# Optimization experiments

Measured on AMD Instinct MI355X. Metric: run time of the kernel, lower is better.

Reference implementation:

```python
import jax, jax.numpy as jnp
import numpy as np

N_NODES = 50000
N_EDGES = 800000
D_FEAT = 128
HIDDEN = 128
N_CLASSES = 40


def setup_inputs() -> dict:
    key = jax.random.key(0)
    ks = jax.random.split(key, 8)
    s = 1.0 / np.sqrt(D_FEAT)
    return {
        "x": jax.random.normal(ks[0], (N_NODES, D_FEAT), jnp.float32),
        "edge_index": jax.random.randint(ks[1], (2, N_EDGES), 0, N_NODES, jnp.int64),
        "Wl0": jax.random.normal(ks[2], (D_FEAT, HIDDEN), jnp.float32) * s,
        "bl0": jnp.zeros((HIDDEN,), jnp.float32),
        "Wr0": jax.random.normal(ks[3], (D_FEAT, HIDDEN), jnp.float32) * s,
        "Wl1": jax.random.normal(ks[4], (HIDDEN, HIDDEN), jnp.float32) * s,
        "bl1": jnp.zeros((HIDDEN,), jnp.float32),
        "Wr1": jax.random.normal(ks[5], (HIDDEN, HIDDEN), jnp.float32) * s,
        "Wl2": jax.random.normal(ks[6], (HIDDEN, N_CLASSES), jnp.float32) * s,
        "bl2": jnp.zeros((N_CLASSES,), jnp.float32),
        "Wr2": jax.random.normal(ks[7], (HIDDEN, N_CLASSES), jnp.float32) * s,
    }


def _sage_conv(x, src, dst, Wl, bl, Wr):
    # PyG SAGEConv (mean aggr): out = lin_l(mean_{j in N(i)} x_j) + lin_r(x_i)
    msg_sum = jax.ops.segment_sum(x[src], dst, num_segments=N_NODES)  # [N, d]
    deg = jax.ops.segment_sum(jnp.ones((src.shape[0],), x.dtype), dst, num_segments=N_NODES)
    mean = msg_sum / jnp.clip(deg, 1.0)[:, None]
    return mean @ Wl + bl + x @ Wr


def reference(x, edge_index, Wl0, bl0, Wr0, Wl1, bl1, Wr1, Wl2, bl2, Wr2):
    src, dst = edge_index[0], edge_index[1]
    h = jax.nn.relu(_sage_conv(x, src, dst, Wl0, bl0, Wr0))
    h = jax.nn.relu(_sage_conv(h, src, dst, Wl1, bl1, Wr1))
    h = jax.nn.relu(_sage_conv(h, src, dst, Wl2, bl2, Wr2))
    # dropout is identity in eval mode
    return jax.nn.log_softmax(h, axis=1)
```

## Files before the change

### kernel.cpp

```cpp
#include <hip/hip_runtime.h>
#include <cstdint>
#include <cstddef>
#include <cmath>

#define N_NODES 50000
#define N_EDGES 800000
#define D_FEAT 128
#define HIDDEN 128
#define N_CLASSES 40

typedef _Float16 half8 __attribute__((ext_vector_type(8)));
typedef _Float16 half4 __attribute__((ext_vector_type(4)));
typedef float f32x4 __attribute__((ext_vector_type(4)));

#define EDGE_BLOCKS 3125
#define CVT_BLOCKS 6250


__global__ __launch_bounds__(256) void k_build(const int* __restrict__ dst, int* __restrict__ deg,
                                               unsigned short* __restrict__ rank,
                                               const float* __restrict__ x, _Float16* __restrict__ xh,
                                               const float* __restrict__ Wl0, const float* __restrict__ Wr0, _Float16* __restrict__ Wc0,
                                               const float* __restrict__ Wl1, const float* __restrict__ Wr1, _Float16* __restrict__ Wc1,
                                               const float* __restrict__ Wl2, const float* __restrict__ Wr2, _Float16* __restrict__ Wc2) {
    int bid = blockIdx.x;
    if (bid < EDGE_BLOCKS) {
        int e = bid * 256 + threadIdx.x;
        int r = atomicAdd(&deg[dst[e]], 1);
        rank[e] = (unsigned short)r;
        return;
    }
    bid -= EDGE_BLOCKS;
    if (bid < CVT_BLOCKS) {
        int i = bid * 256 + threadIdx.x;
        float4 v = *(const float4*)(x + (size_t)i * 4);
        half4 o;
        o[0] = (_Float16)v.x; o[1] = (_Float16)v.y; o[2] = (_Float16)v.z; o[3] = (_Float16)v.w;
        *(half4*)(xh + (size_t)i * 4) = o;
        return;
    }
    bid -= CVT_BLOCKS;
    const float* Wl; const float* Wr; _Float16* dstw; int NF, Nout, cell0;
    if (bid < 16)      { Wl = Wl0; Wr = Wr0; dstw = Wc0; NF = 8; Nout = 128; cell0 = bid * 4; }
    else if (bid < 32) { Wl = Wl1; Wr = Wr1; dstw = Wc1; NF = 8; Nout = 128; cell0 = (bid - 16) * 4; }
    else               { Wl = Wl2; Wr = Wr2; dstw = Wc2; NF = 3; Nout = 40;  cell0 = (bid - 32) * 4; }
    int cell = cell0 + (threadIdx.x >> 6);
    int t = cell / NF;
    int f = cell % NF;
    int l = threadIdx.x & 63;
    int kb = t * 32 + (l >> 4) * 8;
    int n = f * 16 + (l & 15);
    half8 v;
    #pragma unroll
    for (int i = 0; i < 8; ++i) {
        int k = kb + i;
        float w = 0.f;
        if (n < Nout) w = (k < 128) ? Wl[k * Nout + n] : Wr[(k - 128) * Nout + n];
        v[i] = (_Float16)w;
    }
    *(half8*)(dstw + ((size_t)cell * 64 + l) * 8) = v;
}


__global__ __launch_bounds__(1024) void k_scan1(const int* __restrict__ deg, int* __restrict__ offsets,
                                                int* __restrict__ partials) {
    __shared__ int wsums[16];
    int tid = threadIdx.x;
    int g = blockIdx.x * 1024 + tid;
    int v = (g < N_NODES) ? deg[g] : 0;
    int lane = tid & 63;
    int wid = tid >> 6;
    int incl = v;
    #pragma unroll
    for (int off = 1; off < 64; off <<= 1) {
        int t = __shfl_up(incl, off);
        if (lane >= off) incl += t;
    }
    if (lane == 63) wsums[wid] = incl;
    __syncthreads();
    if (wid == 0) {
        int wv = (lane < 16) ? wsums[lane] : 0;
        int wincl = wv;
        #pragma unroll
        for (int off = 1; off < 16; off <<= 1) {
            int t = __shfl_up(wincl, off);
            if (lane >= off) wincl += t;
        }
        if (lane < 16) wsums[lane] = wincl - wv;
    }
    __syncthreads();
    if (g < N_NODES) offsets[g] = wsums[wid] + incl - v;
    if (tid == 1023) partials[blockIdx.x] = wsums[15] + incl;
}

__global__ __launch_bounds__(64) void k_scan2(int* __restrict__ partials, int nParts) {
    int lane = threadIdx.x;
    int v = (lane < nParts) ? partials[lane] : 0;
    int incl = v;
    #pragma unroll
    for (int off = 1; off < 64; off <<= 1) {
        int t = __shfl_up(incl, off);
        if (lane >= off) incl += t;
    }
    if (lane < nParts) partials[lane] = incl - v;
}

__global__ __launch_bounds__(256) void k_scatter(const int* __restrict__ src, const int* __restrict__ dst,
                                                 const int* __restrict__ offsets, const int* __restrict__ partials,
                                                 const unsigned short* __restrict__ rank,
                                                 unsigned short* __restrict__ sorted_src) {
    int e = blockIdx.x * 256 + threadIdx.x;
    if (e < N_EDGES) {
        int d = dst[e];
        int pos = offsets[d] + partials[d >> 10] + (int)rank[e];
        sorted_src[pos] = (unsigned short)src[e];
    }
}


__global__ __launch_bounds__(256) void k_agg_h(const _Float16* __restrict__ feat, const int* __restrict__ offsets,
                                               const int* __restrict__ partials, const int* __restrict__ deg,
                                               const unsigned short* __restrict__ sorted_src,
                                               _Float16* __restrict__ mean) {
    int node = (int)((blockIdx.x * 256 + threadIdx.x) >> 4);
    int cl = threadIdx.x & 15;
    if (node >= N_NODES) return;
    int start = offsets[node] + partials[node >> 10];
    int cnt = deg[node];
    float acc[8] = {0.f, 0.f, 0.f, 0.f, 0.f, 0.f, 0.f, 0.f};
    #pragma unroll 4
    for (int e = 0; e < cnt; ++e) {
        int s = (int)sorted_src[start + e];
        half8 v = *(const half8*)(feat + (size_t)s * 128 + cl * 8);
        #pragma unroll
        for (int q = 0; q < 8; ++q) acc[q] += (float)v[q];
    }
    float r = 1.0f / (float)(cnt > 0 ? cnt : 1);
    half8 o;
    #pragma unroll
    for (int q = 0; q < 8; ++q) o[q] = (_Float16)(acc[q] * r);
    *(half8*)(mean + (size_t)node * 128 + cl * 8) = o;
}


__global__ __launch_bounds__(256) void k_gemm_h(const _Float16* __restrict__ A, const _Float16* __restrict__ B,
                                                const _Float16* __restrict__ Wc, const float* __restrict__ bias,
                                                _Float16* __restrict__ outp) {
    __shared__ _Float16 sA[128 * 128];
    __shared__ _Float16 sB[128 * 128];
    int tid = threadIdx.x;
    int rows0 = blockIdx.x * 128;
    for (int i = 0; i < 8; ++i) {
        int cid = i * 256 + tid;
        int r = cid >> 4;
        int ch = cid & 15;
        int gr = rows0 + r;
        int grc = gr < N_NODES ? gr : N_NODES - 1;
        half8 va = *(const half8*)(A + (size_t)grc * 128 + ch * 8);
        half8 vb = *(const half8*)(B + (size_t)grc * 128 + ch * 8);
        int sch = ch ^ (r & 15);
        *(half8*)(sA + r * 128 + sch * 8) = va;
        *(half8*)(sB + r * 128 + sch * 8) = vb;
    }
    __syncthreads();
    int w = tid >> 6;
    int lane = tid & 63;
    int ln = lane & 15, lg = lane >> 4;
    int r0 = w * 32 + ln;
    int r1 = r0 + 16;
    f32x4 acc[2][8];
    #pragma unroll
    for (int i = 0; i < 2; ++i)
        #pragma unroll
        for (int f = 0; f < 8; ++f) acc[i][f] = (f32x4){0.f, 0.f, 0.f, 0.f};
    #pragma unroll
    for (int t = 0; t < 8; ++t) {
        const _Float16* P = (t < 4) ? sA : sB;
        int ch = (t & 3) * 4 + lg;
        half8 a0 = *(const half8*)(P + r0 * 128 + (ch ^ (r0 & 15)) * 8);
        half8 a1 = *(const half8*)(P + r1 * 128 + (ch ^ (r1 & 15)) * 8);
        #pragma unroll
        for (int f = 0; f < 8; ++f) {
            half8 b = *(const half8*)(Wc + ((size_t)(t * 8 + f) * 64 + lane) * 8);
            acc[0][f] = __builtin_amdgcn_mfma_f32_16x16x32_f16(a0, b, acc[0][f], 0, 0, 0);
            acc[1][f] = __builtin_amdgcn_mfma_f32_16x16x32_f16(a1, b, acc[1][f], 0, 0, 0);
        }
    }
    int rw = rows0 + w * 32;
    #pragma unroll
    for (int mf = 0; mf < 2; ++mf) {
        #pragma unroll
        for (int f = 0; f < 8; ++f) {
            int n = f * 16 + ln;
            float bv = bias[n];
            #pragma unroll
            for (int r = 0; r < 4; ++r) {
                int m = rw + mf * 16 + lg * 4 + r;
                if (m < N_NODES) {
                    float v = fmaxf(acc[mf][f][r] + bv, 0.f);
                    outp[(size_t)m * 128 + n] = (_Float16)v;
                }
            }
        }
    }
}


__global__ __launch_bounds__(256) void k_gemm_f(const _Float16* __restrict__ A, const _Float16* __restrict__ B,
                                                const _Float16* __restrict__ Wc, const float* __restrict__ bias,
                                                float* __restrict__ outp) {
    __shared__ _Float16 sA[128 * 128];
    __shared__ _Float16 sB[128 * 128];
    int tid = threadIdx.x;
    int rows0 = blockIdx.x * 128;
    for (int i = 0; i < 8; ++i) {
        int cid = i * 256 + tid;
        int r = cid >> 4;
        int ch = cid & 15;
        int gr = rows0 + r;
        int grc = gr < N_NODES ? gr : N_NODES - 1;
        half8 va = *(const half8*)(A + (size_t)grc * 128 + ch * 8);
        half8 vb = *(const half8*)(B + (size_t)grc * 128 + ch * 8);
        int sch = ch ^ (r & 15);
        *(half8*)(sA + r * 128 + sch * 8) = va;
        *(half8*)(sB + r * 128 + sch * 8) = vb;
    }
    __syncthreads();
    int w = tid >> 6;
    int lane = tid & 63;
    int ln = lane & 15, lg = lane >> 4;
    int r0 = w * 32 + ln;
    int r1 = r0 + 16;
    f32x4 acc[2][3];
    #pragma unroll
    for (int i = 0; i < 2; ++i)
        #pragma unroll
        for (int f = 0; f < 3; ++f) acc[i][f] = (f32x4){0.f, 0.f, 0.f, 0.f};
    #pragma unroll
    for (int t = 0; t < 8; ++t) {
        const _Float16* P = (t < 4) ? sA : sB;
        int ch = (t & 3) * 4 + lg;
        half8 a0 = *(const half8*)(P + r0 * 128 + (ch ^ (r0 & 15)) * 8);
        half8 a1 = *(const half8*)(P + r1 * 128 + (ch ^ (r1 & 15)) * 8);
        #pragma unroll
        for (int f = 0; f < 3; ++f) {
            half8 b = *(const half8*)(Wc + ((size_t)(t * 3 + f) * 64 + lane) * 8);
            acc[0][f] = __builtin_amdgcn_mfma_f32_16x16x32_f16(a0, b, acc[0][f], 0, 0, 0);
            acc[1][f] = __builtin_amdgcn_mfma_f32_16x16x32_f16(a1, b, acc[1][f], 0, 0, 0);
        }
    }
    float bv[3];
    #pragma unroll
    for (int f = 0; f < 3; ++f) {
        int n = f * 16 + ln;
        bv[f] = (n < N_CLASSES) ? bias[n] : 0.f;
    }
    int rw = rows0 + w * 32;
    #pragma unroll
    for (int mf = 0; mf < 2; ++mf) {
        #pragma unroll
        for (int r = 0; r < 4; ++r) {
            int m = rw + mf * 16 + lg * 4 + r;
            float v[3];
            float vmax = -INFINITY;
            #pragma unroll
            for (int f = 0; f < 3; ++f) {
                int n = f * 16 + ln;
                v[f] = fmaxf(acc[mf][f][r] + bv[f], 0.f);
                if (n < N_CLASSES) vmax = fmaxf(vmax, v[f]);
            }
            #pragma unroll
            for (int off = 1; off < 16; off <<= 1) vmax = fmaxf(vmax, __shfl_xor(vmax, off));
            float s = 0.f;
            #pragma unroll
            for (int f = 0; f < 3; ++f) {
                int n = f * 16 + ln;
                if (n < N_CLASSES) s += expf(v[f] - vmax);
            }
            #pragma unroll
            for (int off = 1; off < 16; off <<= 1) s += __shfl_xor(s, off);
            float lse = vmax + logf(s);
            if (m < N_NODES) {
                #pragma unroll
                for (int f = 0; f < 3; ++f) {
                    int n = f * 16 + ln;
                    if (n < N_CLASSES) outp[(size_t)m * N_CLASSES + n] = v[f] - lse;
                }
            }
        }
    }
}

extern "C" void kernel_launch(void* const* d_in, const int* in_sizes, int n_in,
                              void* d_out, int out_size, void* d_ws, size_t ws_size,
                              hipStream_t stream) {
    const float* x   = (const float*)d_in[0];
    const int*   ei  = (const int*)d_in[1];
    const float* Wl0 = (const float*)d_in[2];
    const float* bl0 = (const float*)d_in[3];
    const float* Wr0 = (const float*)d_in[4];
    const float* Wl1 = (const float*)d_in[5];
    const float* bl1 = (const float*)d_in[6];
    const float* Wr1 = (const float*)d_in[7];
    const float* Wl2 = (const float*)d_in[8];
    const float* bl2 = (const float*)d_in[9];
    const float* Wr2 = (const float*)d_in[10];
    float* out = (float*)d_out;

    const int* src = ei;
    const int* dst = ei + N_EDGES;

    int* offsets  = (int*)d_ws;
    int* deg      = offsets + 50016;
    int* partials = deg + 50016;
    unsigned short* rank   = (unsigned short*)(partials + 64);
    unsigned short* sorted = rank + N_EDGES;
    _Float16* xh  = (_Float16*)(sorted + N_EDGES);
    _Float16* mh  = xh + (size_t)N_NODES * 128;
    _Float16* h0  = mh + (size_t)N_NODES * 128;
    _Float16* h1  = h0 + (size_t)N_NODES * 128;
    _Float16* Wc0 = h1 + (size_t)N_NODES * 128;
    _Float16* Wc1 = Wc0 + 8 * 8 * 64 * 8;
    _Float16* Wc2 = Wc1 + 8 * 8 * 64 * 8;

    hipMemsetAsync(deg, 0, 50016 * sizeof(int), stream);

    const int scanBlocks = (N_NODES + 1023) / 1024;
    k_build<<<EDGE_BLOCKS + CVT_BLOCKS + 38, 256, 0, stream>>>(dst, deg, rank, x, xh,
                                                               Wl0, Wr0, Wc0, Wl1, Wr1, Wc1, Wl2, Wr2, Wc2);
    k_scan1<<<scanBlocks, 1024, 0, stream>>>(deg, offsets, partials);
    k_scan2<<<1, 64, 0, stream>>>(partials, scanBlocks);
    k_scatter<<<EDGE_BLOCKS, 256, 0, stream>>>(src, dst, offsets, partials, rank, sorted);

    const int aggBlocks  = (N_NODES * 16 + 255) / 256;
    const int gemmBlocks = (N_NODES + 127) / 128;

    k_agg_h<<<aggBlocks, 256, 0, stream>>>(xh, offsets, partials, deg, sorted, mh);
    k_gemm_h<<<gemmBlocks, 256, 0, stream>>>(mh, xh, Wc0, bl0, h0);
    k_agg_h<<<aggBlocks, 256, 0, stream>>>(h0, offsets, partials, deg, sorted, mh);
    k_gemm_h<<<gemmBlocks, 256, 0, stream>>>(mh, h0, Wc1, bl1, h1);
    k_agg_h<<<aggBlocks, 256, 0, stream>>>(h1, offsets, partials, deg, sorted, mh);
    k_gemm_f<<<gemmBlocks, 256, 0, stream>>>(mh, h1, Wc2, bl2, out);
}
```

Measured before the change: 279.1 us.

## Replace global atomic degree count with per-block LDS histograms and column scan

Edge ranking moves from global atomics on deg to 64 blocks that each build a shared-memory histogram of destination nodes in two halves, writing per-block counts to a hist matrix. A new column-scan kernel turns the per-block counts into exclusive prefixes and degrees, and the scatter adds the block prefix to the local rank. This removes contended global atomics and the memset, but adds a 64x50000 int histogram write/read, a serial column scan, and only 64 busy blocks for the histogram. The aggregation loop unroll also rises from 4 to 8.

```diff
diff --git a/kernel.cpp b/kernel.cpp
--- a/kernel.cpp
+++ b/kernel.cpp
@@ -13,41 +13,64 @@
 typedef _Float16 half4 __attribute__((ext_vector_type(4)));
 typedef float f32x4 __attribute__((ext_vector_type(4)));
 
-#define EDGE_BLOCKS 3125
-#define CVT_BLOCKS 6250
-
-
-__global__ __launch_bounds__(256) void k_build(const int* __restrict__ dst, int* __restrict__ deg,
-                                               unsigned short* __restrict__ rank,
+#define HB 64
+#define EPB (N_EDGES / HB)
+#define NHALF 25000
+#define CVT1_BLOCKS 1563
+
+
+__global__ __launch_bounds__(1024) void k_hist(const int* __restrict__ dst,
+                                               unsigned short* __restrict__ lrank, int* __restrict__ hist,
                                                const float* __restrict__ x, _Float16* __restrict__ xh,
                                                const float* __restrict__ Wl0, const float* __restrict__ Wr0, _Float16* __restrict__ Wc0,
                                                const float* __restrict__ Wl1, const float* __restrict__ Wr1, _Float16* __restrict__ Wc1,
                                                const float* __restrict__ Wl2, const float* __restrict__ Wr2, _Float16* __restrict__ Wc2) {
+    __shared__ int cnt[NHALF];
     int bid = blockIdx.x;
-    if (bid < EDGE_BLOCKS) {
-        int e = bid * 256 + threadIdx.x;
-        int r = atomicAdd(&deg[dst[e]], 1);
-        rank[e] = (unsigned short)r;
+    int tid = threadIdx.x;
+    if (bid < HB) {
+        int ebase = bid * EPB;
+        #pragma unroll
+        for (int half = 0; half < 2; ++half) {
+            int lo = half * NHALF;
+            for (int i = tid; i < NHALF; i += 1024) cnt[i] = 0;
+            __syncthreads();
+            for (int i = tid; i < EPB; i += 1024) {
+                int d = dst[ebase + i];
+                int dl = d - lo;
+                if ((unsigned)dl < (unsigned)NHALF) {
+                    int r = atomicAdd(&cnt[dl], 1);
+                    lrank[ebase + i] = (unsigned short)r;
+                }
+            }
+            __syncthreads();
+            for (int i = tid; i < NHALF; i += 1024)
+                hist[(size_t)bid * N_NODES + lo + i] = cnt[i];
+            __syncthreads();
+        }
         return;
     }
-    bid -= EDGE_BLOCKS;
-    if (bid < CVT_BLOCKS) {
-        int i = bid * 256 + threadIdx.x;
-        float4 v = *(const float4*)(x + (size_t)i * 4);
-        half4 o;
-        o[0] = (_Float16)v.x; o[1] = (_Float16)v.y; o[2] = (_Float16)v.z; o[3] = (_Float16)v.w;
-        *(half4*)(xh + (size_t)i * 4) = o;
+    bid -= HB;
+    if (bid < CVT1_BLOCKS) {
+        int i = bid * 1024 + tid;
+        if (i < N_NODES * D_FEAT / 4) {
+            float4 v = *(const float4*)(x + (size_t)i * 4);
+            half4 o;
+            o[0] = (_Float16)v.x; o[1] = (_Float16)v.y; o[2] = (_Float16)v.z; o[3] = (_Float16)v.w;
+            *(half4*)(xh + (size_t)i * 4) = o;
+        }
         return;
     }
-    bid -= CVT_BLOCKS;
-    const float* Wl; const float* Wr; _Float16* dstw; int NF, Nout, cell0;
-    if (bid < 16)      { Wl = Wl0; Wr = Wr0; dstw = Wc0; NF = 8; Nout = 128; cell0 = bid * 4; }
-    else if (bid < 32) { Wl = Wl1; Wr = Wr1; dstw = Wc1; NF = 8; Nout = 128; cell0 = (bid - 16) * 4; }
-    else               { Wl = Wl2; Wr = Wr2; dstw = Wc2; NF = 3; Nout = 40;  cell0 = (bid - 32) * 4; }
-    int cell = cell0 + (threadIdx.x >> 6);
-    int t = cell / NF;
-    int f = cell % NF;
-    int l = threadIdx.x & 63;
+    bid -= CVT1_BLOCKS;
+    int cell = bid * 16 + (tid >> 6);
+    if (cell >= 152) return;
+    const float* Wl; const float* Wr; _Float16* dstw; int NF, Nout, c;
+    if (cell < 64)       { Wl = Wl0; Wr = Wr0; dstw = Wc0; NF = 8; Nout = 128; c = cell; }
+    else if (cell < 128) { Wl = Wl1; Wr = Wr1; dstw = Wc1; NF = 8; Nout = 128; c = cell - 64; }
+    else                 { Wl = Wl2; Wr = Wr2; dstw = Wc2; NF = 3; Nout = 40;  c = cell - 128; }
+    int t = c / NF;
+    int f = c % NF;
+    int l = tid & 63;
     int kb = t * 32 + (l >> 4) * 8;
     int n = f * 16 + (l & 15);
     half8 v;
@@ -58,7 +81,22 @@
         if (n < Nout) w = (k < 128) ? Wl[k * Nout + n] : Wr[(k - 128) * Nout + n];
         v[i] = (_Float16)w;
     }
-    *(half8*)(dstw + ((size_t)cell * 64 + l) * 8) = v;
+    *(half8*)(dstw + ((size_t)c * 64 + l) * 8) = v;
+}
+
+
+__global__ __launch_bounds__(1024) void k_colscan(int* __restrict__ hist, int* __restrict__ deg) {
+    int n = blockIdx.x * 1024 + threadIdx.x;
+    if (n >= N_NODES) return;
+    int sum = 0;
+    #pragma unroll 8
+    for (int b = 0; b < HB; ++b) {
+        size_t idx = (size_t)b * N_NODES + n;
+        int v = hist[idx];
+        hist[idx] = sum;
+        sum += v;
+    }
+    deg[n] = sum;
 }
 
 
@@ -105,14 +143,17 @@
     if (lane < nParts) partials[lane] = incl - v;
 }
 
+
 __global__ __launch_bounds__(256) void k_scatter(const int* __restrict__ src, const int* __restrict__ dst,
                                                  const int* __restrict__ offsets, const int* __restrict__ partials,
-                                                 const unsigned short* __restrict__ rank,
+                                                 const int* __restrict__ hist,
+                                                 const unsigned short* __restrict__ lrank,
                                                  unsigned short* __restrict__ sorted_src) {
     int e = blockIdx.x * 256 + threadIdx.x;
     if (e < N_EDGES) {
         int d = dst[e];
-        int pos = offsets[d] + partials[d >> 10] + (int)rank[e];
+        int b = e / EPB;
+        int pos = offsets[d] + partials[d >> 10] + hist[(size_t)b * N_NODES + d] + (int)lrank[e];
         sorted_src[pos] = (unsigned short)src[e];
     }
 }
@@ -128,7 +169,7 @@
     int start = offsets[node] + partials[node >> 10];
     int cnt = deg[node];
     float acc[8] = {0.f, 0.f, 0.f, 0.f, 0.f, 0.f, 0.f, 0.f};
-    #pragma unroll 4
+    #pragma unroll 8
     for (int e = 0; e < cnt; ++e) {
         int s = (int)sorted_src[start + e];
         half8 v = *(const half8*)(feat + (size_t)s * 128 + cl * 8);
@@ -313,8 +354,9 @@
     int* offsets  = (int*)d_ws;
     int* deg      = offsets + 50016;
     int* partials = deg + 50016;
-    unsigned short* rank   = (unsigned short*)(partials + 64);
-    unsigned short* sorted = rank + N_EDGES;
+    int* hist     = partials + 64;
+    unsigned short* lrank  = (unsigned short*)(hist + HB * N_NODES);
+    unsigned short* sorted = lrank + N_EDGES;
     _Float16* xh  = (_Float16*)(sorted + N_EDGES);
     _Float16* mh  = xh + (size_t)N_NODES * 128;
     _Float16* h0  = mh + (size_t)N_NODES * 128;
@@ -323,14 +365,15 @@
     _Float16* Wc1 = Wc0 + 8 * 8 * 64 * 8;
     _Float16* Wc2 = Wc1 + 8 * 8 * 64 * 8;
 
-    hipMemsetAsync(deg, 0, 50016 * sizeof(int), stream);
-
+    const int histGrid = HB + CVT1_BLOCKS + 10;
     const int scanBlocks = (N_NODES + 1023) / 1024;
-    k_build<<<EDGE_BLOCKS + CVT_BLOCKS + 38, 256, 0, stream>>>(dst, deg, rank, x, xh,
-                                                               Wl0, Wr0, Wc0, Wl1, Wr1, Wc1, Wl2, Wr2, Wc2);
+
+    k_hist<<<histGrid, 1024, 0, stream>>>(dst, lrank, hist, x, xh,
+                                          Wl0, Wr0, Wc0, Wl1, Wr1, Wc1, Wl2, Wr2, Wc2);
+    k_colscan<<<scanBlocks, 1024, 0, stream>>>(hist, deg);
     k_scan1<<<scanBlocks, 1024, 0, stream>>>(deg, offsets, partials);
     k_scan2<<<1, 64, 0, stream>>>(partials, scanBlocks);
-    k_scatter<<<EDGE_BLOCKS, 256, 0, stream>>>(src, dst, offsets, partials, rank, sorted);
+    k_scatter<<<(N_EDGES + 255) / 256, 256, 0, stream>>>(src, dst, offsets, partials, hist, lrank, sorted);
 
     const int aggBlocks  = (N_NODES * 16 + 255) / 256;
     const int gemmBlocks = (N_NODES + 127) / 128;
```

After: 277.0 us. About the same (-0.8%).
